# Performance work log

Measured on AMD Instinct MI355X. Metric: run time of the kernel, lower is better.

The kernel has to match this reference:

```python
import jax, jax.numpy as jnp
import numpy as np

D = 1024      # d_model
H = 16        # n_heads
KVH = 4       # num_kv_heads
DH = D // H   # head_dim = 64
CHUNK = 256
SDIM = 128
MG = 8        # m_global
B, T = 4, 4096


def setup_inputs() -> dict:
    key = jax.random.key(0)
    ks = jax.random.split(key, 12)
    s = 0.02
    mk = lambda i, shape: jax.random.normal(ks[i], shape, jnp.float32) * s
    return dict(
        x=jax.random.normal(ks[0], (B, T, D), jnp.float32),
        state=jnp.zeros((B, SDIM), jnp.float32),
        Wq=mk(1, (D, D)), Wk=mk(2, (KVH * DH, D)), Wv=mk(3, (KVH * DH, D)),
        Wo=mk(4, (D, D)), bo=jnp.zeros((D,), jnp.float32),
        ln_attn_g=jnp.ones((D,), jnp.float32), ln_attn_b=jnp.zeros((D,), jnp.float32),
        ln_ffn_g=jnp.ones((D,), jnp.float32), ln_ffn_b=jnp.zeros((D,), jnp.float32),
        W1=mk(5, (4 * D, D)), b1=jnp.zeros((4 * D,), jnp.float32),
        W2=mk(6, (D, 4 * D)), b2=jnp.zeros((D,), jnp.float32),
        Wsp=mk(7, (SDIM, D)), bsp=jnp.zeros((SDIM,), jnp.float32),
        Wsi=mk(8, (D, SDIM)), bsi=jnp.zeros((D,), jnp.float32),
        gtok=mk(9, (MG, D)),
    )


def _ln(x, g, b):
    m = x.mean(-1, keepdims=True)
    v = ((x - m) ** 2).mean(-1, keepdims=True)
    return (x - m) / jnp.sqrt(v + 1e-5) * g + b


def reference(x, state, Wq, Wk, Wv, Wo, bo, ln_attn_g, ln_attn_b,
              ln_ffn_g, ln_ffn_b, W1, b1, W2, b2, Wsp, bsp, Wsi, bsi, gtok):
    Bn, Tn, Dn = x.shape
    nchunks = Tn // CHUNK
    Tc = MG + CHUNK            # tokens per attention call (globals + chunk)
    G = H // KVH               # query heads per KV head
    causal = jnp.tril(jnp.ones((Tc, Tc), bool))
    scale = 1.0 / np.sqrt(DH).astype(np.float32)

    def step(st, chunk):  # st:[B,SDIM], chunk:[B,CHUNK,D]
        h = _ln(chunk, ln_attn_g, ln_attn_b) + (st @ Wsi.T + bsi)[:, None, :]
        h_in = jnp.concatenate([jnp.broadcast_to(gtok, (Bn, MG, Dn)), h], axis=1)
        q = (h_in @ Wq.T).reshape(Bn, Tc, H, DH)
        k = (h_in @ Wk.T).reshape(Bn, Tc, KVH, DH)
        v = (h_in @ Wv.T).reshape(Bn, Tc, KVH, DH)
        # GQA: group query heads over shared KV heads
        qg = q.reshape(Bn, Tc, KVH, G, DH)
        scores = jnp.einsum('bqhgd,bkhd->bhgqk', qg * scale, k)
        scores = jnp.where(causal, scores, -jnp.inf)
        attn = jax.nn.softmax(scores, axis=-1)
        o = jnp.einsum('bhgqk,bkhd->bqhgd', attn, v).reshape(Bn, Tc, Dn)
        y = (o @ Wo.T + bo)[:, MG:, :]
        c = chunk + y
        ff = jax.nn.gelu(_ln(c, ln_ffn_g, ln_ffn_b) @ W1.T + b1, approximate=False) @ W2.T + b2
        c = c + ff
        new_st = c.mean(axis=1) @ Wsp.T + bsp
        return new_st, c

    chunks = x.reshape(Bn, nchunks, CHUNK, Dn).transpose(1, 0, 2, 3)
    final_state, outs = jax.lax.scan(step, state, chunks)
    y_full = outs.transpose(1, 0, 2, 3).reshape(Bn, Tn, Dn)
    return y_full, final_state
```

## Files before the change

### kernel.cpp

```cpp
#include <hip/hip_runtime.h>
#include <hip/hip_bf16.h>

#define Dm    1024
#define Hn    16
#define KVH   4
#define DH    64
#define CHUNK 256
#define SDIM  128
#define MG    8
#define Bn    4
#define Tn    4096
#define TC    264
#define NSTEP 16
#define TD    4194304L

typedef __attribute__((ext_vector_type(8))) short short8;
typedef __attribute__((ext_vector_type(4))) float floatx4;
typedef __hip_bfloat16 bf16;

__device__ __forceinline__ void gl16(const void* g, void* l) {
    using GP = const __attribute__((address_space(1))) char*;
    using LP = __attribute__((address_space(3))) char*;
    __builtin_amdgcn_global_load_lds((GP)g, (LP)l, 16, 0, 0);
}
__device__ __forceinline__ float b2f(short s) {
    unsigned int u = ((unsigned int)(unsigned short)s) << 16;
    float f; __builtin_memcpy(&f, &u, 4); return f;
}
__device__ __forceinline__ short f2b(float f) {
    bf16 h = __float2bfloat16(f);
    short s; __builtin_memcpy(&s, &h, 2); return s;
}


__global__ __launch_bounds__(512) void vcopy_k(const float* __restrict__ s, float* __restrict__ d, int n) {
    int i = blockIdx.x * 512 + threadIdx.x;
    if (i < n) d[i] = s[i];
}

__global__ __launch_bounds__(256) void cvt_bf16_k(const float* __restrict__ s, bf16* __restrict__ d, int n4) {
    int i = blockIdx.x * 256 + threadIdx.x;
    if (i >= n4) return;
    float4 v = ((const float4*)s)[i];
    bf16* o = d + i * 4;
    o[0] = __float2bfloat16(v.x); o[1] = __float2bfloat16(v.y);
    o[2] = __float2bfloat16(v.z); o[3] = __float2bfloat16(v.w);
}

__global__ __launch_bounds__(256) void wsiT_k(const float* __restrict__ Wsi, bf16* __restrict__ WsiT) {
    int idx = blockIdx.x * 256 + threadIdx.x;
    int s = idx >> 10, d = idx & 1023;
    WsiT[idx] = __float2bfloat16(Wsi[d * SDIM + s]);
}

__global__ __launch_bounds__(64) void bfused_k(const bf16* __restrict__ wqkv, const float* __restrict__ bsi,
                                               float* __restrict__ bfused) {
    int n = blockIdx.x * 64 + threadIdx.x;
    const bf16* wr = wqkv + (long)n * 1024;
    float a = 0.f;
    for (int k8 = 0; k8 < 128; ++k8) {
        short8 wv = *(const short8*)(wr + k8 * 8);
#pragma unroll
        for (int e = 0; e < 8; ++e) a += b2f(wv[e]) * bsi[k8 * 8 + e];
    }
    bfused[n] = a;
}

__global__ __launch_bounds__(256) void lng_k(const float* __restrict__ x, const float* __restrict__ gtok,
                                             const float* __restrict__ g, const float* __restrict__ be,
                                             bf16* __restrict__ lnxg, int c0) {
    int bx = blockIdx.x, b = blockIdx.y, tid = threadIdx.x;
    int sl = bx / 264, r = bx - sl * 264;
    bf16* orow = lnxg + (long)((sl * 4 + b) * 264 + r) * 1024 + tid * 4;
    if (r < MG) {
        float4 v = *(const float4*)(gtok + r * 1024 + tid * 4);
        orow[0] = __float2bfloat16(v.x); orow[1] = __float2bfloat16(v.y);
        orow[2] = __float2bfloat16(v.z); orow[3] = __float2bfloat16(v.w);
        return;
    }
    const float* row = x + (long)b * TD + ((long)(c0 + sl) * 256 + (r - MG)) * 1024;
    float4 v = *(const float4*)(row + tid * 4);
    float s = v.x + v.y + v.z + v.w;
    float q = v.x * v.x + v.y * v.y + v.z * v.z + v.w * v.w;
    for (int off = 32; off > 0; off >>= 1) { s += __shfl_down(s, off); q += __shfl_down(q, off); }
    __shared__ float red[10];
    int w = tid >> 6;
    if ((tid & 63) == 0) { red[w] = s; red[4 + w] = q; }
    __syncthreads();
    if (tid == 0) {
        float ts = red[0] + red[1] + red[2] + red[3];
        float tq = red[4] + red[5] + red[6] + red[7];
        float mean = ts * (1.f / Dm);
        float var = tq * (1.f / Dm) - mean * mean;
        red[8] = mean;
        red[9] = rsqrtf(var + 1e-5f);
    }
    __syncthreads();
    float mean = red[8], rstd = red[9];
    int d = tid * 4;
    float4 gv = *(const float4*)(g + d);
    float4 bv = *(const float4*)(be + d);
    orow[0] = __float2bfloat16((v.x - mean) * rstd * gv.x + bv.x);
    orow[1] = __float2bfloat16((v.y - mean) * rstd * gv.y + bv.y);
    orow[2] = __float2bfloat16((v.z - mean) * rstd * gv.z + bv.z);
    orow[3] = __float2bfloat16((v.w - mean) * rstd * gv.w + bv.w);
}

template<int BN>
__global__ __launch_bounds__(256) void gemm64(
    const bf16* __restrict__ A, const bf16* __restrict__ W,
    int M, int N, int K, int kspan,
    bf16* __restrict__ Cb, int ldc, const float* __restrict__ bias, int gelu,
    float* __restrict__ Cpart, long partMN)
{
    constexpr int NSEG = 4 + BN / 16;
    constexpr int SEGW = NSEG / 4;
    constexpr int FC   = BN / 64;
    constexpr int WN   = BN / 4;
    constexpr int HALFB = NSEG * 1024;
    constexpr int PHB   = 2 * HALFB;
    __shared__ short S[PHB];

    int tid = threadIdx.x;
    int w = tid >> 6, l = tid & 63;
    int m0 = blockIdx.y << 6, n0 = blockIdx.x * BN;
    long kb = (long)blockIdx.z * kspan;

    const bf16* gp[SEGW];
    int so[SEGW];
#pragma unroll
    for (int si = 0; si < SEGW; ++si) {
        int s = w + si * 4;
        const bf16* base = (s < 4) ? (A + (long)(m0 + s * 16 + (l >> 2)) * K)
                                   : (W + (long)(n0 + (s - 4) * 16 + (l >> 2)) * K);
        gp[si] = base + ((l & 3) << 3) + kb;
        so[si] = s * 1024 + l * 16;
    }
    char* cS = (char*)S;

    floatx4 acc[4][FC];
#pragma unroll
    for (int t = 0; t < 4; ++t)
#pragma unroll
        for (int u = 0; u < FC; ++u) acc[t][u] = (floatx4){0.f, 0.f, 0.f, 0.f};

    int arow = l & 15;
    int acol = (l >> 4) << 3;
    int np = kspan >> 6;

#define STAGE(p)                                                         \
    {                                                                    \
        int kt_ = (p) << 6;                                              \
        char* b_ = cS + ((p) & 1) * PHB;                                 \
        _Pragma("unroll")                                                \
        for (int si = 0; si < SEGW; ++si) {                              \
            gl16(gp[si] + kt_, b_ + so[si]);                             \
            gl16(gp[si] + kt_ + 32, b_ + HALFB + so[si]);                \
        }                                                                \
    }

    STAGE(0)
    for (int p = 0; p < np; ++p) {
        if (p + 1 < np) {
            STAGE(p + 1)
            if constexpr (SEGW == 2) asm volatile("s_waitcnt vmcnt(4)" ::: "memory");
            else                     asm volatile("s_waitcnt vmcnt(6)" ::: "memory");
        } else {
            asm volatile("s_waitcnt vmcnt(0)" ::: "memory");
        }
        __builtin_amdgcn_s_barrier();
        __builtin_amdgcn_sched_barrier(0);
        const short* buf = S + (p & 1) * (PHB / 2);
#pragma unroll
        for (int kh = 0; kh < 2; ++kh) {
            const short* hb = buf + kh * (HALFB / 2);
            short8 a[4], b[FC];
#pragma unroll
            for (int t = 0; t < 4; ++t)
                a[t] = *(const short8*)&hb[(t * 16 + arow) * 32 + acol];
#pragma unroll
            for (int u = 0; u < FC; ++u)
                b[u] = *(const short8*)&hb[2048 + (w * WN + u * 16 + arow) * 32 + acol];
#pragma unroll
            for (int t = 0; t < 4; ++t)
#pragma unroll
                for (int u = 0; u < FC; ++u)
                    acc[t][u] = __builtin_amdgcn_mfma_f32_16x16x32_bf16(a[t], b[u], acc[t][u], 0, 0, 0);
        }
        __builtin_amdgcn_sched_barrier(0);
        __builtin_amdgcn_s_barrier();
    }
#undef STAGE

    int crow0 = m0 + ((l >> 4) << 2);
    int ccol0 = n0 + w * WN + (l & 15);
    if (Cpart) {
        float* pp = Cpart + (long)blockIdx.z * partMN;
#pragma unroll
        for (int t = 0; t < 4; ++t)
#pragma unroll
            for (int rr = 0; rr < 4; ++rr) {
                int m = crow0 + t * 16 + rr;
                if (m >= M) continue;
#pragma unroll
                for (int u = 0; u < FC; ++u)
                    pp[(long)m * N + ccol0 + u * 16] = acc[t][u][rr];
            }
    } else {
#pragma unroll
        for (int t = 0; t < 4; ++t)
#pragma unroll
            for (int rr = 0; rr < 4; ++rr) {
                int m = crow0 + t * 16 + rr;
                if (m >= M) continue;
                bf16* crow = Cb + (long)m * ldc;
#pragma unroll
                for (int u = 0; u < FC; ++u) {
                    int n = ccol0 + u * 16;
                    float v = acc[t][u][rr];
                    if (bias) v += bias[n];
                    if (gelu) v = 0.5f * v * (1.f + erff(v * 0.70710678118654752f));
                    crow[n] = __float2bfloat16(v);
                }
            }
    }
}

__global__ __launch_bounds__(256) void reduce_ln_k(const float* __restrict__ part,
                                                   const float* __restrict__ bo,
                                                   const float* __restrict__ x,
                                                   float* __restrict__ out, long roff,
                                                   const float* __restrict__ g,
                                                   const float* __restrict__ be,
                                                   bf16* __restrict__ t_ln) {
    int m = blockIdx.x;
    int b = m >> 8, r = m & 255;
    int tid = threadIdx.x;
    long ro = (long)b * TD + (roff + r) * 1024L + tid * 4;
    int pi = m * 256 + tid;
    float4 s  = ((const float4*)part)[pi];
    float4 p2 = ((const float4*)(part + 1048576))[pi];
    float4 bv = ((const float4*)bo)[tid];
    float4 rv = *(const float4*)(x + ro);
    float c0 = s.x + p2.x + bv.x + rv.x;
    float c1 = s.y + p2.y + bv.y + rv.y;
    float c2 = s.z + p2.z + bv.z + rv.z;
    float c3 = s.w + p2.w + bv.w + rv.w;
    *(float4*)(out + ro) = make_float4(c0, c1, c2, c3);
    float sum = c0 + c1 + c2 + c3;
    float sq  = c0 * c0 + c1 * c1 + c2 * c2 + c3 * c3;
    for (int off = 32; off > 0; off >>= 1) { sum += __shfl_down(sum, off); sq += __shfl_down(sq, off); }
    __shared__ float red[10];
    int w = tid >> 6;
    if ((tid & 63) == 0) { red[w] = sum; red[4 + w] = sq; }
    __syncthreads();
    if (tid == 0) {
        float ts = red[0] + red[1] + red[2] + red[3];
        float tq = red[4] + red[5] + red[6] + red[7];
        float mean = ts * (1.f / Dm);
        float var = tq * (1.f / Dm) - mean * mean;
        red[8] = mean;
        red[9] = rsqrtf(var + 1e-5f);
    }
    __syncthreads();
    float mean = red[8], rstd = red[9];
    float4 gv = ((const float4*)g)[tid];
    float4 bev = ((const float4*)be)[tid];
    bf16* orow = t_ln + (long)(b * CHUNK + r) * Dm + tid * 4;
    orow[0] = __float2bfloat16((c0 - mean) * rstd * gv.x + bev.x);
    orow[1] = __float2bfloat16((c1 - mean) * rstd * gv.y + bev.y);
    orow[2] = __float2bfloat16((c2 - mean) * rstd * gv.z + bev.z);
    orow[3] = __float2bfloat16((c3 - mean) * rstd * gv.w + bev.w);
}

__global__ __launch_bounds__(256) void reduce_colpart_k(const float* __restrict__ part,
                                                        const float* __restrict__ bias,
                                                        float* __restrict__ out, long roff,
                                                        float* __restrict__ colp) {
    int b = blockIdx.x, rg = blockIdx.y, tid = threadIdx.x;
    float4 bv = ((const float4*)bias)[tid];
    float4 cs = make_float4(0.f, 0.f, 0.f, 0.f);
#pragma unroll
    for (int r8 = 0; r8 < 8; ++r8) {
        int r = rg * 8 + r8;
        int pi = (b * 256 + r) * 256 + tid;
        float4 s  = ((const float4*)part)[pi];
        float4 p2 = ((const float4*)(part + 1048576))[pi];
        long ro = (long)b * TD + (roff + r) * 1024L + tid * 4;
        float4 rv = *(const float4*)(out + ro);
        float4 v = make_float4(s.x + p2.x + bv.x + rv.x, s.y + p2.y + bv.y + rv.y,
                               s.z + p2.z + bv.z + rv.z, s.w + p2.w + bv.w + rv.w);
        *(float4*)(out + ro) = v;
        cs.x += v.x; cs.y += v.y; cs.z += v.z; cs.w += v.w;
    }
    *(float4*)(colp + ((b * 32 + rg) << 10) + tid * 4) = cs;
}

__global__ __launch_bounds__(256) void state_update_k(const float* __restrict__ colp,
                                                      const float* __restrict__ Wsp,
                                                      const float* __restrict__ bsp,
                                                      float* __restrict__ st) {
    int b = blockIdx.x;
    int tid = threadIdx.x, w = tid >> 6, l = tid & 63;
    int ss = blockIdx.y * 4 + w;
    float4 m[4];
#pragma unroll
    for (int t = 0; t < 4; ++t) m[t] = make_float4(0.f, 0.f, 0.f, 0.f);
    for (int rg = 0; rg < 32; ++rg) {
        const float* pr = colp + ((b * 32 + rg) << 10) + l * 16;
#pragma unroll
        for (int t = 0; t < 4; ++t) {
            float4 v = *(const float4*)(pr + t * 4);
            m[t].x += v.x; m[t].y += v.y; m[t].z += v.z; m[t].w += v.w;
        }
    }
    const float* wr = Wsp + (long)ss * Dm + l * 16;
    float a = 0.f;
#pragma unroll
    for (int t = 0; t < 4; ++t) {
        float4 wv = *(const float4*)(wr + t * 4);
        a += m[t].x * wv.x + m[t].y * wv.y + m[t].z * wv.z + m[t].w * wv.w;
    }
    a *= (1.f / CHUNK);
    for (int off = 32; off > 0; off >>= 1) a += __shfl_down(a, off);
    if (l == 0) st[b * SDIM + ss] = a + bsp[ss];
}

__global__ __launch_bounds__(256) void attn_mfma_k(const bf16* __restrict__ qkv,
                                                   const float* __restrict__ st,
                                                   const bf16* __restrict__ Wf,
                                                   const float* __restrict__ bfused,
                                                   bf16* __restrict__ o_mat) {
    int qc = blockIdx.x, head = blockIdx.y, b = blockIdx.z;
    int kvh = head >> 2;
    int tid = threadIdx.x, w = tid >> 6, l = tid & 63;
    int m16 = l & 15, h4 = l >> 4;

    __shared__ short Qs[64][64];
    __shared__ short Ks[64][64];
    __shared__ short Vt[64][64];
    __shared__ short Ps[4][16][64];
    __shared__ float sq[64], sk[64], sv[64];

    const long rowq0 = (long)b * TC + MG + qc * 64;
    const bf16* kbase = qkv + ((long)b * TC) * 1536 + 1024 + kvh * DH;
    const bf16* vbase = kbase + 256;

    if (tid < 192) {
        int which = tid >> 6, nn = tid & 63;
        int n = (which == 0) ? head * 64 + nn
              : (which == 1) ? 1024 + kvh * 64 + nn
                             : 1280 + kvh * 64 + nn;
        const bf16* wr = Wf + (long)n * SDIM;
        const float* sr = st + b * SDIM;
        float a = bfused[n];
#pragma unroll
        for (int k8 = 0; k8 < 16; ++k8) {
            short8 wv = *(const short8*)(wr + k8 * 8);
#pragma unroll
            for (int e = 0; e < 8; ++e) a += sr[k8 * 8 + e] * b2f(wv[e]);
        }
        if (which == 0) sq[nn] = a; else if (which == 1) sk[nn] = a; else sv[nn] = a;
    }
    __syncthreads();

#pragma unroll
    for (int p = 0; p < 2; ++p) {
        int rr = p * 32 + (tid >> 3);
        int c0 = (tid & 7) * 8;
        short8 v = *(const short8*)(qkv + (rowq0 + rr) * 1536 + head * DH + c0);
        short8 o;
#pragma unroll
        for (int e = 0; e < 8; ++e) o[e] = f2b(b2f(v[e]) + sq[c0 + e]);
        *(short8*)&Qs[rr][c0] = o;
    }

    float a_m[4] = {-1e30f, -1e30f, -1e30f, -1e30f};
    float a_l[4] = {0.f, 0.f, 0.f, 0.f};
    floatx4 acc_o[4];
#pragma unroll
    for (int dt = 0; dt < 4; ++dt) acc_o[dt] = (floatx4){0.f, 0.f, 0.f, 0.f};
    short8 aq[2];

    int qtok0 = MG + qc * 64 + w * 16 + h4 * 4;
    int ntiles = qc + 2;

    for (int t = 0; t < ntiles; ++t) {
        int jt = t * 64;
#pragma unroll
        for (int p = 0; p < 2; ++p) {
            int rr = p * 32 + (tid >> 3);
            int c0 = (tid & 7) * 8;
            int gk = min(jt + rr, TC - 1);
            short8 v = *(const short8*)(kbase + (long)gk * 1536 + c0);
            short8 o;
            if (gk >= MG) {
#pragma unroll
                for (int e = 0; e < 8; ++e) o[e] = f2b(b2f(v[e]) + sk[c0 + e]);
            } else o = v;
            *(short8*)&Ks[rr][c0] = o;
        }
#pragma unroll
        for (int p = 0; p < 2; ++p) {
            int cg = p * 4 + w;
            int gk = min(jt + l, TC - 1);
            short8 vv = *(const short8*)(vbase + (long)gk * 1536 + cg * 8);
            if (gk >= MG) {
#pragma unroll
                for (int e = 0; e < 8; ++e) vv[e] = f2b(b2f(vv[e]) + sv[cg * 8 + e]);
            }
#pragma unroll
            for (int e = 0; e < 8; ++e) Vt[cg * 8 + e][l] = vv[e];
        }
        __syncthreads();
        if (t == 0) {
            aq[0] = *(const short8*)&Qs[w * 16 + m16][h4 * 8];
            aq[1] = *(const short8*)&Qs[w * 16 + m16][32 + h4 * 8];
        }
        floatx4 s[4];
#pragma unroll
        for (int st_ = 0; st_ < 4; ++st_) {
            s[st_] = (floatx4){0.f, 0.f, 0.f, 0.f};
#pragma unroll
            for (int c = 0; c < 2; ++c) {
                short8 kf = *(const short8*)&Ks[st_ * 16 + m16][c * 32 + h4 * 8];
                s[st_] = __builtin_amdgcn_mfma_f32_16x16x32_bf16(aq[c], kf, s[st_], 0, 0, 0);
            }
        }
#pragma unroll
        for (int st_ = 0; st_ < 4; ++st_) {
            int keyg = jt + st_ * 16 + m16;
#pragma unroll
            for (int r = 0; r < 4; ++r) {
                float v = s[st_][r] * 0.125f;
                s[st_][r] = (keyg > qtok0 + r) ? -1e30f : v;
            }
        }
#pragma unroll
        for (int r = 0; r < 4; ++r) {
            float tm = fmaxf(fmaxf(s[0][r], s[1][r]), fmaxf(s[2][r], s[3][r]));
            tm = fmaxf(tm, __shfl_xor(tm, 1));
            tm = fmaxf(tm, __shfl_xor(tm, 2));
            tm = fmaxf(tm, __shfl_xor(tm, 4));
            tm = fmaxf(tm, __shfl_xor(tm, 8));
            float mn = fmaxf(a_m[r], tm);
            float rs = __expf(a_m[r] - mn);
            a_m[r] = mn;
            float ps = 0.f;
#pragma unroll
            for (int st_ = 0; st_ < 4; ++st_) {
                float p = __expf(s[st_][r] - mn);
                s[st_][r] = p;
                ps += p;
            }
            ps += __shfl_xor(ps, 1); ps += __shfl_xor(ps, 2);
            ps += __shfl_xor(ps, 4); ps += __shfl_xor(ps, 8);
            a_l[r] = a_l[r] * rs + ps;
#pragma unroll
            for (int dt = 0; dt < 4; ++dt) acc_o[dt][r] *= rs;
#pragma unroll
            for (int st_ = 0; st_ < 4; ++st_) {
                Ps[w][h4 * 4 + r][st_ * 16 + m16] = f2b(s[st_][r]);
            }
        }
#pragma unroll
        for (int c = 0; c < 2; ++c) {
            short8 ap = *(const short8*)&Ps[w][m16][c * 32 + h4 * 8];
#pragma unroll
            for (int dt = 0; dt < 4; ++dt) {
                short8 vf = *(const short8*)&Vt[dt * 16 + m16][c * 32 + h4 * 8];
                acc_o[dt] = __builtin_amdgcn_mfma_f32_16x16x32_bf16(ap, vf, acc_o[dt], 0, 0, 0);
            }
        }
        __syncthreads();
    }

#pragma unroll
    for (int r = 0; r < 4; ++r) {
        float inv = 1.f / a_l[r];
        long row = (long)b * CHUNK + qc * 64 + w * 16 + h4 * 4 + r;
#pragma unroll
        for (int dt = 0; dt < 4; ++dt)
            o_mat[row * Dm + head * DH + dt * 16 + m16] = __float2bfloat16(acc_o[dt][r] * inv);
    }
}


extern "C" void kernel_launch(void* const* d_in, const int* in_sizes, int n_in,
                              void* d_out, int out_size, void* d_ws, size_t ws_size,
                              hipStream_t stream) {
    const float* x     = (const float*)d_in[0];
    const float* state = (const float*)d_in[1];
    const float* Wq    = (const float*)d_in[2];
    const float* Wk    = (const float*)d_in[3];
    const float* Wv    = (const float*)d_in[4];
    const float* Wo    = (const float*)d_in[5];
    const float* bo    = (const float*)d_in[6];
    const float* lag   = (const float*)d_in[7];
    const float* lab   = (const float*)d_in[8];
    const float* lfg   = (const float*)d_in[9];
    const float* lfb   = (const float*)d_in[10];
    const float* W1    = (const float*)d_in[11];
    const float* b1    = (const float*)d_in[12];
    const float* W2    = (const float*)d_in[13];
    const float* b2    = (const float*)d_in[14];
    const float* Wsp   = (const float*)d_in[15];
    const float* bsp   = (const float*)d_in[16];
    const float* Wsi   = (const float*)d_in[17];
    const float* bsi   = (const float*)d_in[18];
    const float* gtok  = (const float*)d_in[19];

    float* out = (float*)d_out;
    char*  wsb = (char*)d_ws;

    const long stepQ = 4L * TC * 1536;
    const int G = (ws_size >= (size_t)115000000) ? 16 : 4;

    bf16* wqkv   = (bf16*)(wsb);
    bf16* wo     = (bf16*)(wsb + 3145728);
    bf16* w1     = (bf16*)(wsb + 5242880);
    bf16* w2     = (bf16*)(wsb + 13631488);
    bf16* Wfused = (bf16*)(wsb + 22020096);
    bf16* WsiT   = (bf16*)(wsb + 22413312);
    float* bfused= (float*)(wsb + 22675456);
    float* st    = (float*)(wsb + 22681600);
    bf16* qkvg   = (bf16*)(wsb + 22683648);
    char* R2     = wsb + 22683648 + (size_t)G * 3244032;
    bf16* lnxg   = (bf16*)R2;
    bf16* u      = (bf16*)R2;
    float* part  = (float*)(R2 + 8388608);
    char* scrB   = R2 + 16777216;
    bf16* o_mat  = (bf16*)scrB;
    bf16* t_ln   = (bf16*)scrB;
    float* colp  = (float*)scrB;

    vcopy_k<<<1, 512, 0, stream>>>(state, st, 512);
    cvt_bf16_k<<<1024, 256, 0, stream>>>(Wq, wqkv,            262144);
    cvt_bf16_k<<< 256, 256, 0, stream>>>(Wk, wqkv + 1048576,   65536);
    cvt_bf16_k<<< 256, 256, 0, stream>>>(Wv, wqkv + 1310720,   65536);
    cvt_bf16_k<<<1024, 256, 0, stream>>>(Wo, wo,              262144);
    cvt_bf16_k<<<4096, 256, 0, stream>>>(W1, w1,             1048576);
    cvt_bf16_k<<<4096, 256, 0, stream>>>(W2, w2,             1048576);
    wsiT_k<<<512, 256, 0, stream>>>(Wsi, WsiT);
    gemm64<64><<<dim3(2, 24, 1), 256, 0, stream>>>(
        wqkv, WsiT, 1536, 128, 1024, 1024,
        Wfused, 128, nullptr, 0, nullptr, 0L);
    bfused_k<<<24, 64, 0, stream>>>(wqkv, bsi, bfused);

    for (int s = 0; s < NSTEP; ++s) {
        long roff = (long)s * CHUNK;
        if (s % G == 0) {
            lng_k<<<dim3(G * 264, 4), 256, 0, stream>>>(x, gtok, lag, lab, lnxg, s);
            gemm64<128><<<dim3(12, G * 1056 / 64, 1), 256, 0, stream>>>(
                lnxg, wqkv, G * 1056, 1536, 1024, 1024,
                qkvg, 1536, nullptr, 0, nullptr, 0L);
        }
        const bf16* qkv_s = qkvg + (long)(s % G) * stepQ;
        attn_mfma_k<<<dim3(4, 16, 4), 256, 0, stream>>>(qkv_s, st, Wfused, bfused, o_mat);
        gemm64<64><<<dim3(16, 16, 2), 256, 0, stream>>>(
            o_mat, wo, Bn * CHUNK, 1024, 1024, 512,
            nullptr, 0, nullptr, 0, part, 1048576L);
        reduce_ln_k<<<1024, 256, 0, stream>>>(part, bo, x, out, roff, lfg, lfb, t_ln);
        gemm64<128><<<dim3(32, 16, 1), 256, 0, stream>>>(
            t_ln, w1, Bn * CHUNK, 4096, 1024, 1024,
            u, 4096, b1, 1, nullptr, 0L);
        gemm64<64><<<dim3(16, 16, 2), 256, 0, stream>>>(
            u, w2, Bn * CHUNK, 1024, 4096, 2048,
            nullptr, 0, nullptr, 0, part, 1048576L);
        reduce_colpart_k<<<dim3(4, 32), 256, 0, stream>>>(part, b2, out, roff, colp);
        state_update_k<<<dim3(4, 32), 256, 0, stream>>>(colp, Wsp, bsp, st);
    }
    vcopy_k<<<1, 512, 0, stream>>>(st, out + (long)Bn * Tn * Dm, 512);
}
```

Before: 1.522 ms.

## Fuse state update into column reduction and add 128x128 QKV GEMM

Removes the separate state_update kernel. Each reduce_colpart block now multiplies its partial column sums by Wsp and atomically accumulates into a double-buffered next-state vector, which reduce_ln_k seeds with bsp. A new 128x128-tile GEMM with XCD-aware block remapping replaces the 64-row GEMM for the batched QKV projection. This saves one launch per step and improves reuse in the QKV GEMM, at the cost of float atomics that make the sum order nondeterministic. st1 aliases the WsiT region, which is no longer needed after Wfused is computed.

```diff
diff --git a/kernel.cpp b/kernel.cpp
--- a/kernel.cpp
+++ b/kernel.cpp
@@ -106,6 +106,99 @@
     orow[3] = __float2bfloat16((v.w - mean) * rstd * gv.w + bv.w);
 }
 
+__global__ __launch_bounds__(256) void gemm128(
+    const bf16* __restrict__ A, const bf16* __restrict__ W,
+    int M, int N, int K, bf16* __restrict__ Cb, int ldc)
+{
+    __shared__ short As[2][4096];
+    __shared__ short Bs[2][4096];
+    int tid = threadIdx.x;
+    int w = tid >> 6, l = tid & 63;
+    int wr = w >> 1, wc = w & 1;
+
+    int nbx = gridDim.x;
+    int nwg = nbx * gridDim.y;
+    int orig = blockIdx.y * nbx + blockIdx.x;
+    int q = nwg >> 3, r8 = nwg & 7, xcd = orig & 7;
+    int base = (xcd < r8) ? xcd * (q + 1) : r8 * (q + 1) + (xcd - r8) * q;
+    int nid = base + (orig >> 3);
+    int by = nid / nbx, bx = nid - by * nbx;
+    int m0 = by << 7, n0 = bx << 7;
+
+    int r0 = w * 16 + (l >> 2);
+    int kc = (l & 3) << 3;
+    const bf16* pA0 = A + (long)(m0 + r0) * K + kc;
+    const bf16* pA1 = pA0 + (long)64 * K;
+    const bf16* pW0 = W + (long)(n0 + r0) * K + kc;
+    const bf16* pW1 = pW0 + (long)64 * K;
+    int lofs = w * 1024 + l * 16;
+    char* cA = (char*)As;
+    char* cB = (char*)Bs;
+
+    floatx4 acc[4][4];
+#pragma unroll
+    for (int i = 0; i < 4; ++i)
+#pragma unroll
+        for (int j = 0; j < 4; ++j) acc[i][j] = (floatx4){0.f, 0.f, 0.f, 0.f};
+
+    int arow = wr * 64 + (l & 15);
+    int brow = wc * 64 + (l & 15);
+    int acol = (l >> 4) << 3;
+    int nk = K >> 5;
+
+#define STAGE(t)                                            \
+    {                                                       \
+        int kt_ = (t) << 5;                                 \
+        int bo_ = ((t) & 1) * 8192;                         \
+        gl16(pA0 + kt_, cA + bo_ + lofs);                   \
+        gl16(pA1 + kt_, cA + bo_ + 4096 + lofs);            \
+        gl16(pW0 + kt_, cB + bo_ + lofs);                   \
+        gl16(pW1 + kt_, cB + bo_ + 4096 + lofs);            \
+    }
+
+    STAGE(0)
+    for (int i = 0; i < nk; ++i) {
+        if (i + 1 < nk) {
+            STAGE(i + 1)
+            asm volatile("s_waitcnt vmcnt(4)" ::: "memory");
+        } else {
+            asm volatile("s_waitcnt vmcnt(0)" ::: "memory");
+        }
+        __builtin_amdgcn_s_barrier();
+        __builtin_amdgcn_sched_barrier(0);
+        const short* Ab = As[i & 1];
+        const short* Bb = Bs[i & 1];
+        short8 a[4], b[4];
+#pragma unroll
+        for (int t = 0; t < 4; ++t) {
+            a[t] = *(const short8*)&Ab[(arow + t * 16) * 32 + acol];
+            b[t] = *(const short8*)&Bb[(brow + t * 16) * 32 + acol];
+        }
+#pragma unroll
+        for (int ii = 0; ii < 4; ++ii)
+#pragma unroll
+            for (int jj = 0; jj < 4; ++jj)
+                acc[ii][jj] = __builtin_amdgcn_mfma_f32_16x16x32_bf16(a[ii], b[jj], acc[ii][jj], 0, 0, 0);
+        __builtin_amdgcn_sched_barrier(0);
+        __builtin_amdgcn_s_barrier();
+    }
+#undef STAGE
+
+    int crow0 = m0 + wr * 64 + ((l >> 4) << 2);
+    int ccol0 = n0 + wc * 64 + (l & 15);
+#pragma unroll
+    for (int i = 0; i < 4; ++i)
+#pragma unroll
+        for (int rr = 0; rr < 4; ++rr) {
+            int m = crow0 + i * 16 + rr;
+            if (m >= M) continue;
+            bf16* crow = Cb + (long)m * ldc;
+#pragma unroll
+            for (int j = 0; j < 4; ++j)
+                crow[ccol0 + j * 16] = __float2bfloat16(acc[i][j][rr]);
+        }
+}
+
 template<int BN>
 __global__ __launch_bounds__(256) void gemm64(
     const bf16* __restrict__ A, const bf16* __restrict__ W,
@@ -232,10 +325,13 @@
                                                    float* __restrict__ out, long roff,
                                                    const float* __restrict__ g,
                                                    const float* __restrict__ be,
-                                                   bf16* __restrict__ t_ln) {
+                                                   bf16* __restrict__ t_ln,
+                                                   const float* __restrict__ bsp,
+                                                   float* __restrict__ stn) {
     int m = blockIdx.x;
     int b = m >> 8, r = m & 255;
     int tid = threadIdx.x;
+    if (r == 0 && tid < SDIM) stn[b * SDIM + tid] = bsp[tid];
     long ro = (long)b * TD + (roff + r) * 1024L + tid * 4;
     int pi = m * 256 + tid;
     float4 s  = ((const float4*)part)[pi];
@@ -276,8 +372,11 @@
 __global__ __launch_bounds__(256) void reduce_colpart_k(const float* __restrict__ part,
                                                         const float* __restrict__ bias,
                                                         float* __restrict__ out, long roff,
-                                                        float* __restrict__ colp) {
+                                                        const float* __restrict__ Wsp,
+                                                        float* __restrict__ stn) {
     int b = blockIdx.x, rg = blockIdx.y, tid = threadIdx.x;
+    __shared__ float csm[1024];
+    __shared__ float pss[128];
     float4 bv = ((const float4*)bias)[tid];
     float4 cs = make_float4(0.f, 0.f, 0.f, 0.f);
 #pragma unroll
@@ -293,37 +392,22 @@
         *(float4*)(out + ro) = v;
         cs.x += v.x; cs.y += v.y; cs.z += v.z; cs.w += v.w;
     }
-    *(float4*)(colp + ((b * 32 + rg) << 10) + tid * 4) = cs;
-}
-
-__global__ __launch_bounds__(256) void state_update_k(const float* __restrict__ colp,
-                                                      const float* __restrict__ Wsp,
-                                                      const float* __restrict__ bsp,
-                                                      float* __restrict__ st) {
-    int b = blockIdx.x;
-    int tid = threadIdx.x, w = tid >> 6, l = tid & 63;
-    int ss = blockIdx.y * 4 + w;
-    float4 m[4];
-#pragma unroll
-    for (int t = 0; t < 4; ++t) m[t] = make_float4(0.f, 0.f, 0.f, 0.f);
-    for (int rg = 0; rg < 32; ++rg) {
-        const float* pr = colp + ((b * 32 + rg) << 10) + l * 16;
-#pragma unroll
-        for (int t = 0; t < 4; ++t) {
-            float4 v = *(const float4*)(pr + t * 4);
-            m[t].x += v.x; m[t].y += v.y; m[t].z += v.z; m[t].w += v.w;
-        }
-    }
-    const float* wr = Wsp + (long)ss * Dm + l * 16;
-    float a = 0.f;
-#pragma unroll
-    for (int t = 0; t < 4; ++t) {
-        float4 wv = *(const float4*)(wr + t * 4);
-        a += m[t].x * wv.x + m[t].y * wv.y + m[t].z * wv.z + m[t].w * wv.w;
-    }
-    a *= (1.f / CHUNK);
-    for (int off = 32; off > 0; off >>= 1) a += __shfl_down(a, off);
-    if (l == 0) st[b * SDIM + ss] = a + bsp[ss];
+    csm[tid * 4 + 0] = cs.x; csm[tid * 4 + 1] = cs.y;
+    csm[tid * 4 + 2] = cs.z; csm[tid * 4 + 3] = cs.w;
+    __syncthreads();
+    int w = tid >> 6, l = tid & 63;
+#pragma unroll 4
+    for (int i = 0; i < 32; ++i) {
+        int ss = w * 32 + i;
+        const float* wr = Wsp + (long)ss * Dm + l * 16;
+        float p = 0.f;
+#pragma unroll
+        for (int t = 0; t < 16; ++t) p += csm[l * 16 + t] * wr[t];
+        for (int off = 32; off > 0; off >>= 1) p += __shfl_down(p, off);
+        if (l == 0) pss[ss] = p;
+    }
+    __syncthreads();
+    if (tid < SDIM) atomicAdd(stn + b * SDIM + tid, pss[tid] * (1.f / CHUNK));
 }
 
 __global__ __launch_bounds__(256) void attn_mfma_k(const bf16* __restrict__ qkv,
@@ -522,8 +606,9 @@
     bf16* w2     = (bf16*)(wsb + 13631488);
     bf16* Wfused = (bf16*)(wsb + 22020096);
     bf16* WsiT   = (bf16*)(wsb + 22413312);
+    float* st1   = (float*)(wsb + 22413312);
     float* bfused= (float*)(wsb + 22675456);
-    float* st    = (float*)(wsb + 22681600);
+    float* st0   = (float*)(wsb + 22681600);
     bf16* qkvg   = (bf16*)(wsb + 22683648);
     char* R2     = wsb + 22683648 + (size_t)G * 3244032;
     bf16* lnxg   = (bf16*)R2;
@@ -532,9 +617,8 @@
     char* scrB   = R2 + 16777216;
     bf16* o_mat  = (bf16*)scrB;
     bf16* t_ln   = (bf16*)scrB;
-    float* colp  = (float*)scrB;
-
-    vcopy_k<<<1, 512, 0, stream>>>(state, st, 512);
+
+    vcopy_k<<<1, 512, 0, stream>>>(state, st0, 512);
     cvt_bf16_k<<<1024, 256, 0, stream>>>(Wq, wqkv,            262144);
     cvt_bf16_k<<< 256, 256, 0, stream>>>(Wk, wqkv + 1048576,   65536);
     cvt_bf16_k<<< 256, 256, 0, stream>>>(Wv, wqkv + 1310720,   65536);
@@ -547,28 +631,29 @@
         Wfused, 128, nullptr, 0, nullptr, 0L);
     bfused_k<<<24, 64, 0, stream>>>(wqkv, bsi, bfused);
 
+    float* stbuf[2] = { st0, st1 };
     for (int s = 0; s < NSTEP; ++s) {
         long roff = (long)s * CHUNK;
         if (s % G == 0) {
             lng_k<<<dim3(G * 264, 4), 256, 0, stream>>>(x, gtok, lag, lab, lnxg, s);
-            gemm64<128><<<dim3(12, G * 1056 / 64, 1), 256, 0, stream>>>(
-                lnxg, wqkv, G * 1056, 1536, 1024, 1024,
-                qkvg, 1536, nullptr, 0, nullptr, 0L);
+            gemm128<<<dim3(12, G * 1056 / 128), 256, 0, stream>>>(
+                lnxg, wqkv, G * 1056, 1536, 1024, qkvg, 1536);
         }
         const bf16* qkv_s = qkvg + (long)(s % G) * stepQ;
-        attn_mfma_k<<<dim3(4, 16, 4), 256, 0, stream>>>(qkv_s, st, Wfused, bfused, o_mat);
+        const float* stc = stbuf[s & 1];
+        float* stn = stbuf[(s + 1) & 1];
+        attn_mfma_k<<<dim3(4, 16, 4), 256, 0, stream>>>(qkv_s, stc, Wfused, bfused, o_mat);
         gemm64<64><<<dim3(16, 16, 2), 256, 0, stream>>>(
             o_mat, wo, Bn * CHUNK, 1024, 1024, 512,
             nullptr, 0, nullptr, 0, part, 1048576L);
-        reduce_ln_k<<<1024, 256, 0, stream>>>(part, bo, x, out, roff, lfg, lfb, t_ln);
+        reduce_ln_k<<<1024, 256, 0, stream>>>(part, bo, x, out, roff, lfg, lfb, t_ln, bsp, stn);
         gemm64<128><<<dim3(32, 16, 1), 256, 0, stream>>>(
             t_ln, w1, Bn * CHUNK, 4096, 1024, 1024,
             u, 4096, b1, 1, nullptr, 0L);
         gemm64<64><<<dim3(16, 16, 2), 256, 0, stream>>>(
             u, w2, Bn * CHUNK, 1024, 4096, 2048,
             nullptr, 0, nullptr, 0, part, 1048576L);
-        reduce_colpart_k<<<dim3(4, 32), 256, 0, stream>>>(part, b2, out, roff, colp);
-        state_update_k<<<dim3(4, 32), 256, 0, stream>>>(colp, Wsp, bsp, st);
-    }
-    vcopy_k<<<1, 512, 0, stream>>>(st, out + (long)Bn * Tn * Dm, 512);
-}
+        reduce_colpart_k<<<dim3(4, 32), 256, 0, stream>>>(part, b2, out, roff, Wsp, stn);
+    }
+    vcopy_k<<<1, 512, 0, stream>>>(stbuf[0], out + (long)Bn * Tn * Dm, 512);
+}
```

Result: slower. 1.652 ms (+8.5%).
